# Optimization experiments

Measured on AMD Instinct MI355X. Metric: run time of the kernel, lower is better.

Reference implementation:

```python
import jax, jax.numpy as jnp
import numpy as np

RADIUS = 128  # matches init_kwargs


def setup_inputs() -> dict:
    key = jax.random.key(0)
    kq, kk, kv, ke, ks = jax.random.split(key, 5)
    B, S, d = 2, 4096, 64
    num_pos_ids = 2 * RADIUS + 1  # 257
    return {
        "Q": jax.random.normal(kq, (B, S, d), dtype=jnp.float32),
        "K": jax.random.normal(kk, (B, S, d), dtype=jnp.float32),
        "V": jax.random.normal(kv, (B, S, d), dtype=jnp.float32),
        "rel_embeds": jax.random.normal(ke, (num_pos_ids, d), dtype=jnp.float32),
        "segment_ids": jax.random.randint(ks, (S,), 0, 512, dtype=jnp.int64),
    }


def _slided_rel_pos_ids(seq_len: int, radius: int):
    # (i - j) clamped to [-radius, radius], shifted to [0, 2*radius]
    i = jnp.arange(seq_len)
    return jnp.clip(i[None, :] - i[:, None], -radius, radius) + radius  # [S, S]


def reference(Q, K, V, rel_embeds, segment_ids):
    # Q,K,V: [B, S, d]; rel_embeds: [num_pos_ids, d]; segment_ids unused (segmented=False)
    B, S1, d = Q.shape
    normalizer = jnp.asarray(d, Q.dtype) ** 0.5

    Q_rel = jnp.einsum("bsd,pd->bsp", Q, rel_embeds)      # [B, S1, num_pos_ids]
    energy = jnp.einsum("bsd,btd->bst", Q, K)              # [B, S1, S2]

    rel_pos_ids = _slided_rel_pos_ids(S1, RADIUS)          # [S1, S2]
    rel_shift = jnp.take_along_axis(
        Q_rel, jnp.broadcast_to(rel_pos_ids[None], (B, S1, S1)), axis=2
    )  # [B, S1, S2]

    energy = (energy + rel_shift) / normalizer
    attn = jax.nn.softmax(energy, axis=2)
    Z = jnp.einsum("bst,btd->bsd", attn, V)
    return energy, Z
```

## Files before the change

kernel.cpp:

```cpp
#include <hip/hip_runtime.h>

#define S_LEN 4096
#define BATCH 2
#define DIM 64
#define RAD 128
#define NPOS 257
#define KEXT 4416
#define NKT 276
#define QREL_STR 260
#define PSTR 72

typedef short s16x8 __attribute__((ext_vector_type(8)));
typedef short s16x4 __attribute__((ext_vector_type(4)));
typedef float f32x4 __attribute__((ext_vector_type(4)));
typedef unsigned short u16;
typedef unsigned int u32;

__device__ __forceinline__ u16 f2bf(float f) {
  union { float f; u32 u; } v; v.f = f;
  u32 u = v.u;
  return (u16)((u + 0x7FFFu + ((u >> 16) & 1u)) >> 16);
}

__global__ void prep_k2(const float* __restrict__ K, const float* __restrict__ rel,
                        u16* __restrict__ KF) {
  __shared__ float lds[16][65];
  const int b = blockIdx.y;
  const int Ti = blockIdx.x;
  const int tid = threadIdx.x;
  for (int i = tid; i < 1024; i += 128) {
    const int r = i >> 6, c = i & 63;
    const int t = Ti * 16 + r;
    float v = 0.f;
    if (t < S_LEN) v = K[((size_t)b * S_LEN + t) * DIM + c];
    else if (t - S_LEN < NPOS) v = rel[(size_t)(t - S_LEN) * DIM + c];
    lds[r][c] = v;
  }
  __syncthreads();
  const int ks = tid >> 6, lane = tid & 63;
  const int l15 = lane & 15, q4 = lane >> 4;
  s16x8 o;
#pragma unroll
  for (int j = 0; j < 8; ++j) o[j] = (short)f2bf(lds[l15][ks * 32 + q4 * 8 + j]);
  *reinterpret_cast<s16x8*>(KF + (((size_t)(b * NKT + Ti)) * 2 + ks) * 512 + lane * 8) = o;
}

__global__ void prep_v2(const float* __restrict__ V, u16* __restrict__ VF) {
  __shared__ float lds[64][65];
  const int b = blockIdx.y;
  const int T6 = blockIdx.x;
  const int tid = threadIdx.x;
  for (int i = tid; i < 4096; i += 256) {
    const int r = i >> 6, c = i & 63;
    lds[r][c] = V[((size_t)b * S_LEN + T6 * 64 + r) * DIM + c];
  }
  __syncthreads();
  const int dn = tid >> 6, lane = tid & 63;
  const int l15 = lane & 15, q4 = lane >> 4;
#pragma unroll
  for (int ks = 0; ks < 2; ++ks) {
    s16x8 o;
#pragma unroll
    for (int j = 0; j < 8; ++j) o[j] = (short)f2bf(lds[ks * 32 + q4 * 8 + j][dn * 16 + l15]);
    *reinterpret_cast<s16x8*>(
        VF + ((((size_t)(b * 64 + T6)) * 2 + ks) * 4 + dn) * 512 + lane * 8) = o;
  }
}

__launch_bounds__(512, 4)
__global__ void attn_main(const float* __restrict__ Q,
                          const u16* __restrict__ KF,
                          const u16* __restrict__ VF,
                          float* __restrict__ energy,
                          float* __restrict__ Zout) {
  __shared__ float uni[8448];
  __shared__ u16 plds[8 * 16 * PSTR];

  const int tid = threadIdx.x;
  const int lane = tid & 63;
  const int wid = tid >> 6;
  const int l15 = lane & 15, q4 = lane >> 4;
  const int bx = blockIdx.x;
  const int b = bx >> 8;
  const int s0 = (bx & 255) * 16;

  const u16* KFB = KF + (size_t)b * NKT * 2 * 512;
  const u16* VFB = VF + (size_t)b * 64 * 2 * 4 * 512;
  const int lane8 = lane * 8;

  s16x8 qfrag[2];
  {
    const float* qp = Q + ((size_t)b * S_LEN + s0 + l15) * DIM + q4 * 8;
#pragma unroll
    for (int ks = 0; ks < 2; ++ks) {
      f32x4 a = *reinterpret_cast<const f32x4*>(qp + ks * 32);
      f32x4 c = *reinterpret_cast<const f32x4*>(qp + ks * 32 + 4);
      s16x8 f;
#pragma unroll
      for (int j = 0; j < 4; ++j) { f[j] = (short)f2bf(a[j]); f[4 + j] = (short)f2bf(c[j]); }
      qfrag[ks] = f;
    }
  }

  for (int pt = wid; pt < 5; pt += 8) {
    f32x4 acc[4] = {};
#pragma unroll
    for (int ks = 0; ks < 2; ++ks)
#pragma unroll
      for (int nf = 0; nf < 4; ++nf) {
        s16x8 kf = *reinterpret_cast<const s16x8*>(
            KFB + ((size_t)(256 + pt * 4 + nf) * 2 + ks) * 512 + lane8);
        acc[nf] = __builtin_amdgcn_mfma_f32_16x16x32_bf16(kf, qfrag[ks], acc[nf], 0, 0, 0);
      }
#pragma unroll
    for (int nf = 0; nf < 4; ++nf)
#pragma unroll
      for (int reg = 0; reg < 4; ++reg) {
        int p = pt * 64 + nf * 16 + q4 * 4 + reg;
        if (p < NPOS) uni[l15 * QREL_STR + p] = acc[nf][reg];
      }
  }
  __syncthreads();

  const float c8lo = uni[l15 * QREL_STR + 0] * 0.125f;
  const float c8hi = uni[l15 * QREL_STR + 256] * 0.125f;

  const int qglob = s0 + l15;
  const int qoff = l15 * QREL_STR + RAD;
  u16* pw = plds + wid * 16 * PSTR;
  float* erow = energy + ((size_t)b * S_LEN + qglob) * S_LEN;

  float mprev = -INFINITY, lsum = 0.f;
  f32x4 zacc[4] = {};

  for (int it = 0; it < 8; ++it) {
    const int t0 = wid * 512 + it * 64;
    const int ti4 = t0 >> 4;
    const int t6 = t0 >> 6;

    f32x4 acc[4] = {};
#pragma unroll
    for (int ks = 0; ks < 2; ++ks)
#pragma unroll
      for (int nf = 0; nf < 4; ++nf) {
        s16x8 kf = *reinterpret_cast<const s16x8*>(
            KFB + ((size_t)(ti4 + nf) * 2 + ks) * 512 + lane8);
        acc[nf] = __builtin_amdgcn_mfma_f32_16x16x32_bf16(kf, qfrag[ks], acc[nf], 0, 0, 0);
      }

    s16x8 vf[2][4];
#pragma unroll
    for (int ks = 0; ks < 2; ++ks)
#pragma unroll
      for (int dn = 0; dn < 4; ++dn)
        vf[ks][dn] = *reinterpret_cast<const s16x8*>(
            VFB + (((size_t)t6 * 2 + ks) * 4 + dn) * 512 + lane8);

    float mloc = -INFINITY;
    if (t0 >= s0 + 143) {
#pragma unroll
      for (int nf = 0; nf < 4; ++nf)
#pragma unroll
        for (int reg = 0; reg < 4; ++reg) {
          float e = fmaf(acc[nf][reg], 0.125f, c8hi);
          acc[nf][reg] = e;
          mloc = fmaxf(mloc, e);
        }
    } else if (t0 <= s0 - 191) {
#pragma unroll
      for (int nf = 0; nf < 4; ++nf)
#pragma unroll
        for (int reg = 0; reg < 4; ++reg) {
          float e = fmaf(acc[nf][reg], 0.125f, c8lo);
          acc[nf][reg] = e;
          mloc = fmaxf(mloc, e);
        }
    } else {
#pragma unroll
      for (int nf = 0; nf < 4; ++nf) {
        const int tb = t0 + nf * 16 + q4 * 4;
#pragma unroll
        for (int reg = 0; reg < 4; ++reg) {
          int p = tb + reg - qglob;
          p = (p < -RAD) ? -RAD : (p > RAD ? RAD : p);
          float e = (acc[nf][reg] + uni[qoff + p]) * 0.125f;
          acc[nf][reg] = e;
          mloc = fmaxf(mloc, e);
        }
      }
    }

#pragma unroll
    for (int nf = 0; nf < 4; ++nf)
      __builtin_nontemporal_store(
          acc[nf], reinterpret_cast<f32x4*>(erow + t0 + nf * 16 + q4 * 4));

    if (__all(mloc <= mprev)) {
    } else {
      mloc = fmaxf(mloc, __shfl_xor(mloc, 16));
      mloc = fmaxf(mloc, __shfl_xor(mloc, 32));
      const float mn = fmaxf(mprev, mloc);
      const float alpha = __expf(mprev - mn);
      mprev = mn;
      lsum *= alpha;
#pragma unroll
      for (int dn = 0; dn < 4; ++dn) zacc[dn] *= alpha;
    }

    float rs = 0.f;
#pragma unroll
    for (int nf = 0; nf < 4; ++nf) {
      float p0 = __expf(acc[nf][0] - mprev);
      float p1 = __expf(acc[nf][1] - mprev);
      float p2 = __expf(acc[nf][2] - mprev);
      float p3 = __expf(acc[nf][3] - mprev);
      rs += (p0 + p1) + (p2 + p3);
      union { u32 w[2]; s16x4 v; } pk;
      asm("v_cvt_pk_bf16_f32 %0, %1, %2" : "=v"(pk.w[0]) : "v"(p0), "v"(p1));
      asm("v_cvt_pk_bf16_f32 %0, %1, %2" : "=v"(pk.w[1]) : "v"(p2), "v"(p3));
      *reinterpret_cast<s16x4*>(pw + l15 * PSTR + nf * 16 + q4 * 4) = pk.v;
    }
    rs += __shfl_xor(rs, 16);
    rs += __shfl_xor(rs, 32);
    lsum += rs;

#pragma unroll
    for (int ks = 0; ks < 2; ++ks) {
      s16x8 pf = *reinterpret_cast<const s16x8*>(pw + l15 * PSTR + ks * 32 + q4 * 8);
#pragma unroll
      for (int dn = 0; dn < 4; ++dn)
        zacc[dn] = __builtin_amdgcn_mfma_f32_16x16x32_bf16(vf[ks][dn], pf, zacc[dn], 0, 0, 0);
    }
  }

  __syncthreads();
#pragma unroll
  for (int dn = 0; dn < 4; ++dn)
    *reinterpret_cast<f32x4*>(&uni[(wid * 16 + l15) * 64 + dn * 16 + q4 * 4]) = zacc[dn];
  if (q4 == 0) {
    uni[8192 + wid * 16 + l15] = mprev;
    uni[8320 + wid * 16 + l15] = lsum;
  }
  __syncthreads();

  {
    const int r0 = tid >> 6, d = tid & 63;
#pragma unroll
    for (int rr = 0; rr < 2; ++rr) {
      const int r = rr * 8 + r0;
      float mf = -INFINITY;
#pragma unroll
      for (int w = 0; w < 8; ++w) mf = fmaxf(mf, uni[8192 + w * 16 + r]);
      float lf = 0.f, z = 0.f;
#pragma unroll
      for (int w = 0; w < 8; ++w) {
        const float sc = __expf(uni[8192 + w * 16 + r] - mf);
        lf += uni[8320 + w * 16 + r] * sc;
        z  += uni[(w * 16 + r) * 64 + d] * sc;
      }
      Zout[((size_t)b * S_LEN + s0 + r) * DIM + d] = z / lf;
    }
  }
}

extern "C" void kernel_launch(void* const* d_in, const int* in_sizes, int n_in,
                              void* d_out, int out_size, void* d_ws, size_t ws_size,
                              hipStream_t stream) {
  const float* Q   = (const float*)d_in[0];
  const float* K   = (const float*)d_in[1];
  const float* V   = (const float*)d_in[2];
  const float* rel = (const float*)d_in[3];

  u16* KF = (u16*)d_ws;
  u16* VF = KF + (size_t)BATCH * NKT * 2 * 512;

  float* energy = (float*)d_out;
  float* Zout   = energy + (size_t)BATCH * S_LEN * S_LEN;

  prep_k2<<<dim3(NKT, BATCH), 128, 0, stream>>>(K, rel, KF);
  prep_v2<<<dim3(S_LEN / 64, BATCH), 256, 0, stream>>>(V, VF);
  attn_main<<<dim3(BATCH * (S_LEN / 16)), 512, 0, stream>>>(Q, KF, VF, energy, Zout);
}
```

Baseline: 52.82 us.

## Stage energy tile in LDS for coalesced row stores and P reuse

Each wave now writes its energy tile to an LDS staging buffer (padded stride 67). It then reads the tile back twice: once to compute the softmax probabilities directly in the MFMA B-fragment layout, which removes the separate P round-trip through LDS, and once to issue row-contiguous 64-float nontemporal stores to global energy instead of scattered 16-byte column chunks. The Q·rel table is stored as bf16 in LDS to fit the staging buffer. This cuts the precision of the relative-position term, which risks accuracy in the energy output, and it adds LDS traffic. The Zbuf reduction reuses the staging buffer, which needs 8448 floats while the buffer holds 8576, so it fits.

```diff
diff --git a/kernel.cpp b/kernel.cpp
--- a/kernel.cpp
+++ b/kernel.cpp
@@ -8,10 +8,9 @@
 #define KEXT 4416
 #define NKT 276
 #define QREL_STR 260
-#define PSTR 72
+#define ESTR 67
 
 typedef short s16x8 __attribute__((ext_vector_type(8)));
-typedef short s16x4 __attribute__((ext_vector_type(4)));
 typedef float f32x4 __attribute__((ext_vector_type(4)));
 typedef unsigned short u16;
 typedef unsigned int u32;
@@ -20,6 +19,9 @@
   union { float f; u32 u; } v; v.f = f;
   u32 u = v.u;
   return (u16)((u + 0x7FFFu + ((u >> 16) & 1u)) >> 16);
+}
+__device__ __forceinline__ float bf2f(u16 h) {
+  union { u32 u; float f; } v; v.u = ((u32)h) << 16; return v.f;
 }
 
 __global__ void prep_k2(const float* __restrict__ K, const float* __restrict__ rel,
@@ -73,8 +75,8 @@
                           const u16* __restrict__ VF,
                           float* __restrict__ energy,
                           float* __restrict__ Zout) {
-  __shared__ float uni[8448];
-  __shared__ u16 plds[8 * 16 * PSTR];
+  __shared__ u16 qrel_bf[16 * QREL_STR];
+  __shared__ float estage[8 * 16 * ESTR];
 
   const int tid = threadIdx.x;
   const int lane = tid & 63;
@@ -117,18 +119,18 @@
 #pragma unroll
       for (int reg = 0; reg < 4; ++reg) {
         int p = pt * 64 + nf * 16 + q4 * 4 + reg;
-        if (p < NPOS) uni[l15 * QREL_STR + p] = acc[nf][reg];
-      }
-  }
-  __syncthreads();
-
-  const float c8lo = uni[l15 * QREL_STR + 0] * 0.125f;
-  const float c8hi = uni[l15 * QREL_STR + 256] * 0.125f;
+        if (p < NPOS) qrel_bf[l15 * QREL_STR + p] = f2bf(acc[nf][reg]);
+      }
+  }
+  __syncthreads();
+
+  const float c8lo = bf2f(qrel_bf[l15 * QREL_STR + 0]) * 0.125f;
+  const float c8hi = bf2f(qrel_bf[l15 * QREL_STR + 256]) * 0.125f;
 
   const int qglob = s0 + l15;
   const int qoff = l15 * QREL_STR + RAD;
-  u16* pw = plds + wid * 16 * PSTR;
-  float* erow = energy + ((size_t)b * S_LEN + qglob) * S_LEN;
+  float* ew = estage + wid * 16 * ESTR;
+  float* eblk = energy + ((size_t)b * S_LEN + s0) * S_LEN;
 
   float mprev = -INFINITY, lsum = 0.f;
   f32x4 zacc[4] = {};
@@ -183,17 +185,15 @@
         for (int reg = 0; reg < 4; ++reg) {
           int p = tb + reg - qglob;
           p = (p < -RAD) ? -RAD : (p > RAD ? RAD : p);
-          float e = (acc[nf][reg] + uni[qoff + p]) * 0.125f;
+          float e = (acc[nf][reg] + bf2f(qrel_bf[qoff + p])) * 0.125f;
           acc[nf][reg] = e;
           mloc = fmaxf(mloc, e);
         }
       }
     }
-
 #pragma unroll
     for (int nf = 0; nf < 4; ++nf)
-      __builtin_nontemporal_store(
-          acc[nf], reinterpret_cast<f32x4*>(erow + t0 + nf * 16 + q4 * 4));
+      *reinterpret_cast<f32x4*>(ew + l15 * ESTR + nf * 16 + q4 * 4) = acc[nf];
 
     if (__all(mloc <= mprev)) {
     } else {
@@ -207,39 +207,56 @@
       for (int dn = 0; dn < 4; ++dn) zacc[dn] *= alpha;
     }
 
+    asm volatile("s_waitcnt lgkmcnt(0)" ::: "memory");
+
     float rs = 0.f;
-#pragma unroll
-    for (int nf = 0; nf < 4; ++nf) {
-      float p0 = __expf(acc[nf][0] - mprev);
-      float p1 = __expf(acc[nf][1] - mprev);
-      float p2 = __expf(acc[nf][2] - mprev);
-      float p3 = __expf(acc[nf][3] - mprev);
-      rs += (p0 + p1) + (p2 + p3);
-      union { u32 w[2]; s16x4 v; } pk;
+    s16x8 pf[2];
+#pragma unroll
+    for (int ks = 0; ks < 2; ++ks) {
+      f32x4 ea = *reinterpret_cast<const f32x4*>(ew + l15 * ESTR + ks * 32 + q4 * 8);
+      f32x4 eb = *reinterpret_cast<const f32x4*>(ew + l15 * ESTR + ks * 32 + q4 * 8 + 4);
+      float p0 = __expf(ea[0] - mprev), p1 = __expf(ea[1] - mprev);
+      float p2 = __expf(ea[2] - mprev), p3 = __expf(ea[3] - mprev);
+      float p4 = __expf(eb[0] - mprev), p5 = __expf(eb[1] - mprev);
+      float p6 = __expf(eb[2] - mprev), p7 = __expf(eb[3] - mprev);
+      rs += ((p0 + p1) + (p2 + p3)) + ((p4 + p5) + (p6 + p7));
+      union { u32 w[4]; s16x8 v; } pk;
       asm("v_cvt_pk_bf16_f32 %0, %1, %2" : "=v"(pk.w[0]) : "v"(p0), "v"(p1));
       asm("v_cvt_pk_bf16_f32 %0, %1, %2" : "=v"(pk.w[1]) : "v"(p2), "v"(p3));
-      *reinterpret_cast<s16x4*>(pw + l15 * PSTR + nf * 16 + q4 * 4) = pk.v;
+      asm("v_cvt_pk_bf16_f32 %0, %1, %2" : "=v"(pk.w[2]) : "v"(p4), "v"(p5));
+      asm("v_cvt_pk_bf16_f32 %0, %1, %2" : "=v"(pk.w[3]) : "v"(p6), "v"(p7));
+      pf[ks] = pk.v;
     }
     rs += __shfl_xor(rs, 16);
     rs += __shfl_xor(rs, 32);
     lsum += rs;
 
 #pragma unroll
-    for (int ks = 0; ks < 2; ++ks) {
-      s16x8 pf = *reinterpret_cast<const s16x8*>(pw + l15 * PSTR + ks * 32 + q4 * 8);
+    for (int ks = 0; ks < 2; ++ks)
 #pragma unroll
       for (int dn = 0; dn < 4; ++dn)
-        zacc[dn] = __builtin_amdgcn_mfma_f32_16x16x32_bf16(vf[ks][dn], pf, zacc[dn], 0, 0, 0);
-    }
-  }
-
-  __syncthreads();
+        zacc[dn] = __builtin_amdgcn_mfma_f32_16x16x32_bf16(vf[ks][dn], pf[ks], zacc[dn], 0, 0, 0);
+
+    {
+      const int hi = lane >> 4, m16 = lane & 15;
+#pragma unroll
+      for (int j = 0; j < 4; ++j) {
+        const int r = j * 4 + hi;
+        f32x4 v = *reinterpret_cast<const f32x4*>(ew + r * ESTR + m16 * 4);
+        __builtin_nontemporal_store(
+            v, reinterpret_cast<f32x4*>(eblk + (size_t)r * S_LEN + t0 + m16 * 4));
+      }
+    }
+  }
+
+  __syncthreads();
+  float* Zbuf = estage;
 #pragma unroll
   for (int dn = 0; dn < 4; ++dn)
-    *reinterpret_cast<f32x4*>(&uni[(wid * 16 + l15) * 64 + dn * 16 + q4 * 4]) = zacc[dn];
+    *reinterpret_cast<f32x4*>(&Zbuf[(wid * 16 + l15) * 64 + dn * 16 + q4 * 4]) = zacc[dn];
   if (q4 == 0) {
-    uni[8192 + wid * 16 + l15] = mprev;
-    uni[8320 + wid * 16 + l15] = lsum;
+    Zbuf[8192 + wid * 16 + l15] = mprev;
+    Zbuf[8320 + wid * 16 + l15] = lsum;
   }
   __syncthreads();
 
@@ -250,13 +267,13 @@
       const int r = rr * 8 + r0;
       float mf = -INFINITY;
 #pragma unroll
-      for (int w = 0; w < 8; ++w) mf = fmaxf(mf, uni[8192 + w * 16 + r]);
+      for (int w = 0; w < 8; ++w) mf = fmaxf(mf, Zbuf[8192 + w * 16 + r]);
       float lf = 0.f, z = 0.f;
 #pragma unroll
       for (int w = 0; w < 8; ++w) {
-        const float sc = __expf(uni[8192 + w * 16 + r] - mf);
-        lf += uni[8320 + w * 16 + r] * sc;
-        z  += uni[(w * 16 + r) * 64 + d] * sc;
+        const float sc = __expf(Zbuf[8192 + w * 16 + r] - mf);
+        lf += Zbuf[8320 + w * 16 + r] * sc;
+        z  += Zbuf[(w * 16 + r) * 64 + d] * sc;
       }
       Zout[((size_t)b * S_LEN + s0 + r) * DIM + d] = z / lf;
     }
```

Result: slower. 65.88 us (+24.7%).
